# Kernel tuning notes

Hardware: AMD Instinct MI355X
Metric: run time of the kernel (lower is better)

Reference implementation:

```python
import jax, jax.numpy as jnp
import numpy as np

B, N, D, L = 8, 2048, 256, 2  # batch, node_size, in_dim==mem_dim, num_layers


def setup_inputs() -> dict:
    key = jax.random.key(0)
    k_nodes, k_adj, k_w0, k_b0, k_wr, k_br = jax.random.split(key, 6)
    nodes = jax.random.normal(k_nodes, (B, N, D), dtype=jnp.float32)
    adj = jax.random.uniform(k_adj, (B, N, N), dtype=jnp.float32)
    s = 1.0 / np.sqrt(D)
    W0_w = jax.random.uniform(k_w0, (L, D, D), dtype=jnp.float32, minval=-s, maxval=s)
    W0_b = jax.random.uniform(k_b0, (L, D), dtype=jnp.float32, minval=-s, maxval=s)
    Wr_w = jax.random.uniform(k_wr, (L, D, D), dtype=jnp.float32, minval=-s, maxval=s)
    Wr_b = jax.random.uniform(k_br, (L, D), dtype=jnp.float32, minval=-s, maxval=s)
    return {"nodes": nodes, "adj": adj, "W0_w": W0_w, "W0_b": W0_b,
            "Wr_w": Wr_w, "Wr_b": Wr_b}


def reference(nodes, adj, W0_w, W0_b, Wr_w, Wr_b):
    # denom[b] = row-sum of adj[b] + 1  -> [B, N, 1]
    denom = jnp.sum(adj, axis=2, keepdims=True) + 1.0
    x = nodes  # dropout is identity in eval mode
    outputs = x
    for l in range(L):
        # W_r branch: aggregate neighbor-transformed features
        xWr = jnp.einsum('bnd,md->bnm', x, Wr_w[l]) + Wr_b[l]   # [B,N,D]
        AxW = jnp.einsum('bnk,bkd->bnd', adj, xWr)              # sparse mm equiv
        # W_0 self branch, fused norm + relu
        xW0 = jnp.einsum('bnd,md->bnm', x, W0_w[l]) + W0_b[l]
        x = jax.nn.relu((AxW + xW0) / denom)
    return outputs + x
```

## Files before the change

### kernel.cpp

```cpp
#include <hip/hip_runtime.h>
#include <hip/hip_fp8.h>

constexpr int B = 8;
constexpr int N = 2048;
constexpr int D = 256;
constexpr int L = 2;
constexpr int M = B * N;

typedef __bf16 bf16x8 __attribute__((ext_vector_type(8)));
typedef float  f32x4  __attribute__((ext_vector_type(4)));
typedef float  f32x16 __attribute__((ext_vector_type(16)));
typedef int    i32x4  __attribute__((ext_vector_type(4)));
typedef int    i32x8  __attribute__((ext_vector_type(8)));

static __device__ __forceinline__ unsigned short f2bf(float f) {
    union { float f; unsigned u; } v; v.f = f;
    unsigned r = v.u + 0x7fffu + ((v.u >> 16) & 1u);
    return (unsigned short)(r >> 16);
}

static __device__ __forceinline__ unsigned char f2fp8(float f) {
    __hip_fp8_e4m3 v(f);
    return (unsigned char)v.__x;
}

static __device__ __forceinline__ void gload16(const void* g, void* l) {
    __builtin_amdgcn_global_load_lds(
        (__attribute__((address_space(1))) void*)(g),
        (__attribute__((address_space(3))) void*)(l),
        16, 0, 0);
}

__global__ __launch_bounds__(256)
void prep_kernel(const float* __restrict__ adj,
                 const float* __restrict__ nodes,
                 const float* __restrict__ W0_w, const float* __restrict__ Wr_w,
                 unsigned char* __restrict__ adj8,
                 float* __restrict__ rdenom, float* __restrict__ rowsum,
                 unsigned short* __restrict__ nodesbf,
                 unsigned char* __restrict__ nodesT8,
                 unsigned short* __restrict__ W0b, unsigned short* __restrict__ Wrb) {
    __shared__ unsigned char T8[64][68];
    const int bx = blockIdx.x;
    const int t  = threadIdx.x;
    if (bx < 4096) {
        const int wave = t >> 6;
        const int lane = t & 63;
        const int row  = bx * 4 + wave;
        const float4* p = (const float4*)(adj + (size_t)row * N);
        uchar4* q = (uchar4*)(adj8 + (size_t)row * N);
        float s = 0.f;
        #pragma unroll
        for (int i = 0; i < 8; ++i) {
            float4 v = p[lane + i * 64];
            s += (v.x + v.y) + (v.z + v.w);
            uchar4 o;
            o.x = f2fp8(v.x); o.y = f2fp8(v.y); o.z = f2fp8(v.z); o.w = f2fp8(v.w);
            q[lane + i * 64] = o;
        }
        #pragma unroll
        for (int off = 32; off > 0; off >>= 1) s += __shfl_down(s, off);
        if (lane == 0) {
            rowsum[row] = s;
            rdenom[row] = 1.0f / (s + 1.0f);
        }
    } else if (bx < 4096 + 1024) {
        const int idx = bx - 4096;
        const int b   = idx >> 7;
        const int rem = idx & 127;
        const int n0  = (rem >> 2) * 64;
        const int d0  = (rem & 3) * 64;
        const int r   = t >> 2;
        const int c4  = t & 3;
        const float*    src = nodes   + ((size_t)b * N + n0) * D + d0;
        unsigned short* dst = nodesbf + ((size_t)b * N + n0) * D + d0;
        #pragma unroll
        for (int rep = 0; rep < 4; ++rep) {
            const int fc = c4 + rep * 4;
            float4 v = *(const float4*)(src + (size_t)r * D + fc * 4);
            ushort4 o;
            o.x = f2bf(v.x); o.y = f2bf(v.y); o.z = f2bf(v.z); o.w = f2bf(v.w);
            *(ushort4*)(dst + (size_t)r * D + fc * 4) = o;
            uchar4 o8;
            o8.x = f2fp8(v.x); o8.y = f2fp8(v.y); o8.z = f2fp8(v.z); o8.w = f2fp8(v.w);
            *(uchar4*)&T8[r][fc * 4] = o8;
        }
        __syncthreads();
        unsigned char* dstT = nodesT8 + ((size_t)b * D + d0) * N + n0;
        #pragma unroll
        for (int rep = 0; rep < 4; ++rep) {
            const int nc = c4 + rep * 4;
            uchar4 o;
            o.x = T8[nc * 4 + 0][r];
            o.y = T8[nc * 4 + 1][r];
            o.z = T8[nc * 4 + 2][r];
            o.w = T8[nc * 4 + 3][r];
            *(uchar4*)(dstT + (size_t)r * N + nc * 4) = o;
        }
    } else {
        const int i = (bx - 5120) * 256 + t;
        float4 a = ((const float4*)W0_w)[i];
        ushort4 o0; o0.x = f2bf(a.x); o0.y = f2bf(a.y); o0.z = f2bf(a.z); o0.w = f2bf(a.w);
        ((ushort4*)W0b)[i] = o0;
        float4 c = ((const float4*)Wr_w)[i];
        ushort4 o1; o1.x = f2bf(c.x); o1.y = f2bf(c.y); o1.z = f2bf(c.z); o1.w = f2bf(c.w);
        ((ushort4*)Wrb)[i] = o1;
    }
}

__global__ __launch_bounds__(256)
void big_mfma_kernel(const unsigned char* __restrict__ adj8,
                     const unsigned char* __restrict__ xT8,
                     unsigned short* __restrict__ ypart) {
    __shared__ __align__(16) unsigned char As[2 * 2048];
    __shared__ __align__(16) unsigned char Bs[4 * 2048];

    const int z     = blockIdx.z;
    const int b     = z & 7;
    const int split = z >> 3;
    const int n0    = blockIdx.x * 128;
    const int m0    = blockIdx.y * 64;
    const int t     = threadIdx.x;
    const int w     = t >> 6;
    const int lane  = t & 63;
    const int r32   = lane & 31;
    const int h32   = lane >> 5;
    const int wr    = w & 1;
    const int wc    = w >> 1;
    const int kbase = split * (N / 2);

    const unsigned char* Ab = adj8 + (size_t)b * N * N + kbase;
    const unsigned char* Bb = xT8  + (size_t)b * D * N + kbase;

    const unsigned char* gA =
        Ab + (size_t)(m0 + (w >> 1) * 32 + r32) * N + h32 * 32 + (w & 1) * 16;
    unsigned char* lA = &As[(w >> 1) * 2048 + (w & 1) * 1024];
    const unsigned char* gB =
        Bb + (size_t)(n0 + w * 32 + r32) * N + h32 * 32;
    unsigned char* lB0 = &Bs[w * 2048];
    unsigned char* lB1 = &Bs[w * 2048 + 1024];

    f32x16 acc[2];
    #pragma unroll
    for (int j = 0; j < 2; ++j)
        #pragma unroll
        for (int e = 0; e < 16; ++e) acc[j][e] = 0.f;

    const int la = lane * 16;

    for (int k0 = 0; k0 < N / 2; k0 += 64) {
        __syncthreads();
        gload16(gA + k0,      lA);
        gload16(gB + k0,      lB0);
        gload16(gB + k0 + 16, lB1);
        __syncthreads();

        i32x4 alo = *(const i32x4*)&As[wr * 2048 + la];
        i32x4 ahi = *(const i32x4*)&As[wr * 2048 + 1024 + la];
        i32x8 af;
        af[0] = alo[0]; af[1] = alo[1]; af[2] = alo[2]; af[3] = alo[3];
        af[4] = ahi[0]; af[5] = ahi[1]; af[6] = ahi[2]; af[7] = ahi[3];

        #pragma unroll
        for (int j = 0; j < 2; ++j) {
            const int sb = wc * 2 + j;
            i32x4 blo = *(const i32x4*)&Bs[sb * 2048 + la];
            i32x4 bhi = *(const i32x4*)&Bs[sb * 2048 + 1024 + la];
            i32x8 bf;
            bf[0] = blo[0]; bf[1] = blo[1]; bf[2] = blo[2]; bf[3] = blo[3];
            bf[4] = bhi[0]; bf[5] = bhi[1]; bf[6] = bhi[2]; bf[7] = bhi[3];
            acc[j] = __builtin_amdgcn_mfma_scale_f32_32x32x64_f8f6f4(
                af, bf, acc[j],
                0 , 0 ,
                0, 0x7f7f7f7f ,
                0, 0x7f7f7f7f );
        }
    }

    unsigned short* yb = ypart + ((size_t)split * M + (size_t)b * N) * D;
    #pragma unroll
    for (int j = 0; j < 2; ++j) {
        #pragma unroll
        for (int r = 0; r < 16; ++r) {
            const int row = (r & 3) + 8 * (r >> 2) + 4 * h32;
            const int m   = m0 + wr * 32 + row;
            const int d   = n0 + wc * 64 + j * 32 + r32;
            yb[(size_t)m * D + d] = f2bf(acc[j][r]);
        }
    }
}

__global__ __launch_bounds__(256)
void small_mfma_kernel(const unsigned short* __restrict__ y0,
                       const unsigned short* __restrict__ y1,
                       const unsigned short* __restrict__ x,
                       const unsigned short* __restrict__ Wrb,
                       const unsigned short* __restrict__ W0b,
                       const float* __restrict__ br,
                       const float* __restrict__ b0,
                       const float* __restrict__ rdenom,
                       const float* __restrict__ rowsum,
                       const float* __restrict__ nodesf,
                       unsigned short* __restrict__ xout,
                       unsigned char* __restrict__ xoutT8,
                       float* __restrict__ out) {
    __shared__ __align__(16) unsigned short As[16 * 512];
    __shared__ __align__(16) unsigned short Bs[8 * 512];

    const int n0   = blockIdx.x * 64;
    const int m0   = blockIdx.y * 128;
    const int t    = threadIdx.x;
    const int w    = t >> 6;
    const int lane = t & 63;
    const int lrow = lane & 15;
    const int lk   = (lane >> 4) * 8;

    const size_t aRow0 = (size_t)(m0 + (2 * w + 0) * 16 + lrow) * D + lk;
    const size_t aRow1 = (size_t)(m0 + (2 * w + 1) * 16 + lrow) * D + lk;
    const size_t bRow  = (size_t)(n0 + w * 16 + lrow) * D + lk;

    f32x4 acc[4][2];
    const f32x4 zero = {0.f, 0.f, 0.f, 0.f};
    #pragma unroll
    for (int i = 0; i < 4; ++i)
        #pragma unroll
        for (int j = 0; j < 2; ++j) acc[i][j] = zero;

    #pragma unroll
    for (int s = 0; s < 3; ++s) {
        const unsigned short* Asrc = (s == 0) ? y0 : (s == 1) ? y1 : x;
        const unsigned short* Bsrc = (s < 2) ? Wrb : W0b;
        #pragma unroll
        for (int kk = 0; kk < D; kk += 64) {
            __syncthreads();
            gload16(Asrc + aRow0 + kk,      &As[((2 * w + 0) * 2 + 0) * 512]);
            gload16(Asrc + aRow0 + kk + 32, &As[((2 * w + 0) * 2 + 1) * 512]);
            gload16(Asrc + aRow1 + kk,      &As[((2 * w + 1) * 2 + 0) * 512]);
            gload16(Asrc + aRow1 + kk + 32, &As[((2 * w + 1) * 2 + 1) * 512]);
            gload16(Bsrc + bRow + kk,       &Bs[(w * 2 + 0) * 512]);
            gload16(Bsrc + bRow + kk + 32,  &Bs[(w * 2 + 1) * 512]);
            __syncthreads();
            #pragma unroll
            for (int kc = 0; kc < 2; ++kc) {
                bf16x8 a[4], bb[2];
                #pragma unroll
                for (int i = 0; i < 4; ++i)
                    a[i] = *(const bf16x8*)&As[((((w & 1) * 4 + i) * 2) + kc) * 512 + lane * 8];
                #pragma unroll
                for (int j = 0; j < 2; ++j)
                    bb[j] = *(const bf16x8*)&Bs[((((w >> 1) * 2 + j) * 2) + kc) * 512 + lane * 8];
                #pragma unroll
                for (int i = 0; i < 4; ++i)
                    #pragma unroll
                    for (int j = 0; j < 2; ++j)
                        acc[i][j] = __builtin_amdgcn_mfma_f32_16x16x32_bf16(
                            a[i], bb[j], acc[i][j], 0, 0, 0);
            }
        }
    }

    const int col  = lane & 15;
    const int quad = lane >> 4;
    #pragma unroll
    for (int i = 0; i < 4; ++i) {
        const int mBase = m0 + (w & 1) * 64 + i * 16 + quad * 4;
        float rd[4], ss[4];
        #pragma unroll
        for (int r = 0; r < 4; ++r) {
            rd[r] = rdenom[mBase + r];
            ss[r] = rowsum[mBase + r];
        }
        #pragma unroll
        for (int j = 0; j < 2; ++j) {
            const int jj = n0 + (w >> 1) * 32 + j * 16 + col;
            const float bj = b0[jj];
            const float bv = br[jj];
            if (out) {
                #pragma unroll
                for (int r = 0; r < 4; ++r) {
                    const size_t idx = (size_t)(mBase + r) * D + jj;
                    float v = (acc[i][j][r] + bj + bv * ss[r]) * rd[r];
                    out[idx] = nodesf[idx] + fmaxf(v, 0.f);
                }
            } else {
                float v0 = fmaxf((acc[i][j][0] + bj + bv * ss[0]) * rd[0], 0.f);
                float v1 = fmaxf((acc[i][j][1] + bj + bv * ss[1]) * rd[1], 0.f);
                float v2 = fmaxf((acc[i][j][2] + bj + bv * ss[2]) * rd[2], 0.f);
                float v3 = fmaxf((acc[i][j][3] + bj + bv * ss[3]) * rd[3], 0.f);
                xout[(size_t)(mBase + 0) * D + jj] = f2bf(v0);
                xout[(size_t)(mBase + 1) * D + jj] = f2bf(v1);
                xout[(size_t)(mBase + 2) * D + jj] = f2bf(v2);
                xout[(size_t)(mBase + 3) * D + jj] = f2bf(v3);
                uchar4 o8;
                o8.x = f2fp8(v0); o8.y = f2fp8(v1); o8.z = f2fp8(v2); o8.w = f2fp8(v3);
                const int bb_  = m0 >> 11;
                const int nloc = mBase & (N - 1);
                *(uchar4*)&xoutT8[((size_t)bb_ * D + jj) * N + nloc] = o8;
            }
        }
    }
}

extern "C" void kernel_launch(void* const* d_in, const int* in_sizes, int n_in,
                              void* d_out, int out_size, void* d_ws, size_t ws_size,
                              hipStream_t stream) {
    const float* nodes = (const float*)d_in[0];
    const float* adj   = (const float*)d_in[1];
    const float* W0_w  = (const float*)d_in[2];
    const float* W0_b  = (const float*)d_in[3];
    const float* Wr_w  = (const float*)d_in[4];
    const float* Wr_b  = (const float*)d_in[5];
    float* out = (float*)d_out;

    unsigned char*  adj8    = (unsigned char*)d_ws;
    unsigned char*  xT8     = adj8 + (size_t)B * N * N;
    unsigned short* nodesbf = (unsigned short*)(xT8 + (size_t)B * D * N);
    unsigned short* ybuf    = nodesbf + (size_t)M * D;
    unsigned short* x1      = ybuf + (size_t)2 * M * D;
    unsigned short* Wrb     = x1 + (size_t)M * D;
    unsigned short* W0b     = Wrb + (size_t)L * D * D;
    float* rdenom = (float*)(W0b + (size_t)L * D * D);
    float* rowsum = rdenom + M;

    prep_kernel<<<dim3(5248), 256, 0, stream>>>(
        adj, nodes, W0_w, Wr_w,
        adj8, rdenom, rowsum, nodesbf, xT8, W0b, Wrb);

    unsigned short* y0 = ybuf;
    unsigned short* y1 = ybuf + (size_t)M * D;

    big_mfma_kernel<<<dim3(D / 128, N / 64, 2 * B), 256, 0, stream>>>(adj8, xT8, ybuf);
    small_mfma_kernel<<<dim3(D / 64, M / 128), 256, 0, stream>>>(
        y0, y1, nodesbf, Wrb, W0b, Wr_b, W0_b, rdenom, rowsum,
        nullptr, x1, xT8, nullptr);

    big_mfma_kernel<<<dim3(D / 128, N / 64, 2 * B), 256, 0, stream>>>(adj8, xT8, ybuf);
    small_mfma_kernel<<<dim3(D / 64, M / 128), 256, 0, stream>>>(
        y0, y1, x1, Wrb + D * D, W0b + D * D, Wr_b + D, W0_b + D, rdenom, rowsum,
        nodes, nullptr, nullptr, out);
}
```

Baseline: 325.6 us.

## Double-buffer LDS loads in both MFMA kernels and use packed fp8 conversion

Both GEMM kernels now keep two LDS buffers. Each loop step issues the async global-to-LDS loads for the next tile, waits only on the previous batch with a vmcnt count, and then computes, so memory latency overlaps with MFMA work. FP8 quantisation in the prep and epilogue paths now uses the hardware packed cvt_pk_fp8_f32 instruction and writes 32-bit words instead of scalar byte conversions. The cost is twice the LDS footprint, which may lower occupancy, and the hand-written vmcnt accounting is fragile if the number of issued loads per stage changes.

```diff
diff --git a/kernel.cpp b/kernel.cpp
--- a/kernel.cpp
+++ b/kernel.cpp
@@ -19,9 +19,22 @@
     return (unsigned short)(r >> 16);
 }
 
+static __device__ __forceinline__ unsigned short f2fp8x2(float a, float b) {
+#if __has_builtin(__builtin_amdgcn_cvt_pk_fp8_f32)
+    return (unsigned short)(__builtin_amdgcn_cvt_pk_fp8_f32(a, b, 0, false) & 0xffff);
+#else
+    __hip_fp8_e4m3 va(a), vb(b);
+    return (unsigned short)((unsigned)va.__x | ((unsigned)vb.__x << 8));
+#endif
+}
+
 static __device__ __forceinline__ unsigned char f2fp8(float f) {
+#if __has_builtin(__builtin_amdgcn_cvt_pk_fp8_f32)
+    return (unsigned char)(__builtin_amdgcn_cvt_pk_fp8_f32(f, f, 0, false) & 0xff);
+#else
     __hip_fp8_e4m3 v(f);
     return (unsigned char)v.__x;
+#endif
 }
 
 static __device__ __forceinline__ void gload16(const void* g, void* l) {
@@ -48,15 +61,15 @@
         const int lane = t & 63;
         const int row  = bx * 4 + wave;
         const float4* p = (const float4*)(adj + (size_t)row * N);
-        uchar4* q = (uchar4*)(adj8 + (size_t)row * N);
+        unsigned* q = (unsigned*)(adj8 + (size_t)row * N);
         float s = 0.f;
         #pragma unroll
         for (int i = 0; i < 8; ++i) {
             float4 v = p[lane + i * 64];
             s += (v.x + v.y) + (v.z + v.w);
-            uchar4 o;
-            o.x = f2fp8(v.x); o.y = f2fp8(v.y); o.z = f2fp8(v.z); o.w = f2fp8(v.w);
-            q[lane + i * 64] = o;
+            unsigned word = (unsigned)f2fp8x2(v.x, v.y)
+                          | ((unsigned)f2fp8x2(v.z, v.w) << 16);
+            q[lane + i * 64] = word;
         }
         #pragma unroll
         for (int off = 32; off > 0; off >>= 1) s += __shfl_down(s, off);
@@ -81,9 +94,9 @@
             ushort4 o;
             o.x = f2bf(v.x); o.y = f2bf(v.y); o.z = f2bf(v.z); o.w = f2bf(v.w);
             *(ushort4*)(dst + (size_t)r * D + fc * 4) = o;
-            uchar4 o8;
-            o8.x = f2fp8(v.x); o8.y = f2fp8(v.y); o8.z = f2fp8(v.z); o8.w = f2fp8(v.w);
-            *(uchar4*)&T8[r][fc * 4] = o8;
+            unsigned word = (unsigned)f2fp8x2(v.x, v.y)
+                          | ((unsigned)f2fp8x2(v.z, v.w) << 16);
+            *(unsigned*)&T8[r][fc * 4] = word;
         }
         __syncthreads();
         unsigned char* dstT = nodesT8 + ((size_t)b * D + d0) * N + n0;
@@ -112,8 +125,8 @@
 void big_mfma_kernel(const unsigned char* __restrict__ adj8,
                      const unsigned char* __restrict__ xT8,
                      unsigned short* __restrict__ ypart) {
-    __shared__ __align__(16) unsigned char As[2 * 2048];
-    __shared__ __align__(16) unsigned char Bs[4 * 2048];
+    __shared__ __align__(16) unsigned char As[2][4096];
+    __shared__ __align__(16) unsigned char Bs[2][8192];
 
     const int z     = blockIdx.z;
     const int b     = z & 7;
@@ -134,11 +147,10 @@
 
     const unsigned char* gA =
         Ab + (size_t)(m0 + (w >> 1) * 32 + r32) * N + h32 * 32 + (w & 1) * 16;
-    unsigned char* lA = &As[(w >> 1) * 2048 + (w & 1) * 1024];
+    const int lAoff = (w >> 1) * 2048 + (w & 1) * 1024;
     const unsigned char* gB =
         Bb + (size_t)(n0 + w * 32 + r32) * N + h32 * 32;
-    unsigned char* lB0 = &Bs[w * 2048];
-    unsigned char* lB1 = &Bs[w * 2048 + 1024];
+    const int lBoff = w * 2048;
 
     f32x16 acc[2];
     #pragma unroll
@@ -148,15 +160,26 @@
 
     const int la = lane * 16;
 
-    for (int k0 = 0; k0 < N / 2; k0 += 64) {
-        __syncthreads();
-        gload16(gA + k0,      lA);
-        gload16(gB + k0,      lB0);
-        gload16(gB + k0 + 16, lB1);
-        __syncthreads();
-
-        i32x4 alo = *(const i32x4*)&As[wr * 2048 + la];
-        i32x4 ahi = *(const i32x4*)&As[wr * 2048 + 1024 + la];
+    gload16(gA,      &As[0][lAoff]);
+    gload16(gB,      &Bs[0][lBoff]);
+    gload16(gB + 16, &Bs[0][lBoff + 1024]);
+
+    for (int step = 0; step < 16; ++step) {
+        const int cur = step & 1;
+        if (step < 15) {
+            const int kn = (step + 1) * 64;
+            gload16(gA + kn,      &As[cur ^ 1][lAoff]);
+            gload16(gB + kn,      &Bs[cur ^ 1][lBoff]);
+            gload16(gB + kn + 16, &Bs[cur ^ 1][lBoff + 1024]);
+            asm volatile("s_waitcnt vmcnt(3)" ::: "memory");
+        } else {
+            asm volatile("s_waitcnt vmcnt(0)" ::: "memory");
+        }
+        __builtin_amdgcn_s_barrier();
+        __builtin_amdgcn_sched_barrier(0);
+
+        i32x4 alo = *(const i32x4*)&As[cur][wr * 2048 + la];
+        i32x4 ahi = *(const i32x4*)&As[cur][wr * 2048 + 1024 + la];
         i32x8 af;
         af[0] = alo[0]; af[1] = alo[1]; af[2] = alo[2]; af[3] = alo[3];
         af[4] = ahi[0]; af[5] = ahi[1]; af[6] = ahi[2]; af[7] = ahi[3];
@@ -164,8 +187,8 @@
         #pragma unroll
         for (int j = 0; j < 2; ++j) {
             const int sb = wc * 2 + j;
-            i32x4 blo = *(const i32x4*)&Bs[sb * 2048 + la];
-            i32x4 bhi = *(const i32x4*)&Bs[sb * 2048 + 1024 + la];
+            i32x4 blo = *(const i32x4*)&Bs[cur][sb * 2048 + la];
+            i32x4 bhi = *(const i32x4*)&Bs[cur][sb * 2048 + 1024 + la];
             i32x8 bf;
             bf[0] = blo[0]; bf[1] = blo[1]; bf[2] = blo[2]; bf[3] = blo[3];
             bf[4] = bhi[0]; bf[5] = bhi[1]; bf[6] = bhi[2]; bf[7] = bhi[3];
@@ -175,6 +198,8 @@
                 0, 0x7f7f7f7f ,
                 0, 0x7f7f7f7f );
         }
+        __builtin_amdgcn_sched_barrier(0);
+        __builtin_amdgcn_s_barrier();
     }
 
     unsigned short* yb = ypart + ((size_t)split * M + (size_t)b * N) * D;
@@ -204,8 +229,8 @@
                        unsigned short* __restrict__ xout,
                        unsigned char* __restrict__ xoutT8,
                        float* __restrict__ out) {
-    __shared__ __align__(16) unsigned short As[16 * 512];
-    __shared__ __align__(16) unsigned short Bs[8 * 512];
+    __shared__ __align__(16) unsigned short As[2][8192];
+    __shared__ __align__(16) unsigned short Bs[2][4096];
 
     const int n0   = blockIdx.x * 64;
     const int m0   = blockIdx.y * 128;
@@ -226,37 +251,50 @@
         #pragma unroll
         for (int j = 0; j < 2; ++j) acc[i][j] = zero;
 
-    #pragma unroll
-    for (int s = 0; s < 3; ++s) {
-        const unsigned short* Asrc = (s == 0) ? y0 : (s == 1) ? y1 : x;
-        const unsigned short* Bsrc = (s < 2) ? Wrb : W0b;
-        #pragma unroll
-        for (int kk = 0; kk < D; kk += 64) {
-            __syncthreads();
-            gload16(Asrc + aRow0 + kk,      &As[((2 * w + 0) * 2 + 0) * 512]);
-            gload16(Asrc + aRow0 + kk + 32, &As[((2 * w + 0) * 2 + 1) * 512]);
-            gload16(Asrc + aRow1 + kk,      &As[((2 * w + 1) * 2 + 0) * 512]);
-            gload16(Asrc + aRow1 + kk + 32, &As[((2 * w + 1) * 2 + 1) * 512]);
-            gload16(Bsrc + bRow + kk,       &Bs[(w * 2 + 0) * 512]);
-            gload16(Bsrc + bRow + kk + 32,  &Bs[(w * 2 + 1) * 512]);
-            __syncthreads();
+    auto stage = [&](int q, int buf) {
+        const int seg = q >> 2;
+        const int kk  = (q & 3) * 64;
+        const unsigned short* Asrc = (seg == 0) ? y0 : (seg == 1) ? y1 : x;
+        const unsigned short* Bsrc = (seg < 2) ? Wrb : W0b;
+        gload16(Asrc + aRow0 + kk,      &As[buf][(4 * w + 0) * 512]);
+        gload16(Asrc + aRow0 + kk + 32, &As[buf][(4 * w + 1) * 512]);
+        gload16(Asrc + aRow1 + kk,      &As[buf][(4 * w + 2) * 512]);
+        gload16(Asrc + aRow1 + kk + 32, &As[buf][(4 * w + 3) * 512]);
+        gload16(Bsrc + bRow + kk,       &Bs[buf][(2 * w + 0) * 512]);
+        gload16(Bsrc + bRow + kk + 32,  &Bs[buf][(2 * w + 1) * 512]);
+    };
+
+    stage(0, 0);
+
+    for (int q = 0; q < 12; ++q) {
+        const int cur = q & 1;
+        if (q < 11) {
+            stage(q + 1, cur ^ 1);
+            asm volatile("s_waitcnt vmcnt(6)" ::: "memory");
+        } else {
+            asm volatile("s_waitcnt vmcnt(0)" ::: "memory");
+        }
+        __builtin_amdgcn_s_barrier();
+        __builtin_amdgcn_sched_barrier(0);
+
+        #pragma unroll
+        for (int kc = 0; kc < 2; ++kc) {
+            bf16x8 a[4], bb[2];
             #pragma unroll
-            for (int kc = 0; kc < 2; ++kc) {
-                bf16x8 a[4], bb[2];
-                #pragma unroll
-                for (int i = 0; i < 4; ++i)
-                    a[i] = *(const bf16x8*)&As[((((w & 1) * 4 + i) * 2) + kc) * 512 + lane * 8];
+            for (int i = 0; i < 4; ++i)
+                a[i] = *(const bf16x8*)&As[cur][((((w & 1) * 4 + i) * 2) + kc) * 512 + lane * 8];
+            #pragma unroll
+            for (int j = 0; j < 2; ++j)
+                bb[j] = *(const bf16x8*)&Bs[cur][((((w >> 1) * 2 + j) * 2) + kc) * 512 + lane * 8];
+            #pragma unroll
+            for (int i = 0; i < 4; ++i)
                 #pragma unroll
                 for (int j = 0; j < 2; ++j)
-                    bb[j] = *(const bf16x8*)&Bs[((((w >> 1) * 2 + j) * 2) + kc) * 512 + lane * 8];
-                #pragma unroll
-                for (int i = 0; i < 4; ++i)
-                    #pragma unroll
-                    for (int j = 0; j < 2; ++j)
-                        acc[i][j] = __builtin_amdgcn_mfma_f32_16x16x32_bf16(
-                            a[i], bb[j], acc[i][j], 0, 0, 0);
-            }
-        }
+                    acc[i][j] = __builtin_amdgcn_mfma_f32_16x16x32_bf16(
+                        a[i], bb[j], acc[i][j], 0, 0, 0);
+        }
+        __builtin_amdgcn_sched_barrier(0);
+        __builtin_amdgcn_s_barrier();
     }
 
     const int col  = lane & 15;
@@ -291,11 +329,11 @@
                 xout[(size_t)(mBase + 1) * D + jj] = f2bf(v1);
                 xout[(size_t)(mBase + 2) * D + jj] = f2bf(v2);
                 xout[(size_t)(mBase + 3) * D + jj] = f2bf(v3);
-                uchar4 o8;
-                o8.x = f2fp8(v0); o8.y = f2fp8(v1); o8.z = f2fp8(v2); o8.w = f2fp8(v3);
+                unsigned word = (unsigned)f2fp8x2(v0, v1)
+                              | ((unsigned)f2fp8x2(v2, v3) << 16);
                 const int bb_  = m0 >> 11;
                 const int nloc = mBase & (N - 1);
-                *(uchar4*)&xoutT8[((size_t)bb_ * D + jj) * N + nloc] = o8;
+                *(unsigned*)&xoutT8[((size_t)bb_ * D + jj) * N + nloc] = word;
             }
         }
     }
```

After: 327.0 us. Within noise of the previous version (+0.4%).
